# Kernel optimization log

Measured on AMD Instinct MI355X. Metric: run time of the kernel, lower is better.

## Reference

```python
import jax, jax.numpy as jnp
import numpy as np

B, L, H, V = 16, 1024, 512, 32000
HALF = H // 2
ALPHA = 0.95
EPS_NORM = 1e-12
EPS_LN = 1e-5


def setup_inputs() -> dict:
    key = jax.random.key(0)
    ks = jax.random.split(key, 12)
    s = 0.02
    return {
        "seq": jax.random.randint(ks[0], (B, L), 0, V),
        "embed": jax.random.normal(ks[1], (V, H), jnp.float32) * s,
        "ff_w1": jax.random.normal(ks[2], (2 * H, H), jnp.float32) * s,
        "ff_b1": jnp.zeros((2 * H,), jnp.float32),
        "ff_w2": jax.random.normal(ks[3], (H, 2 * H), jnp.float32) * s,
        "ff_b2": jnp.zeros((H,), jnp.float32),
        "gamma": jnp.ones((H,), jnp.float32),
        "beta": jnp.zeros((H,), jnp.float32),
        "sem_w": jax.random.normal(ks[4], (HALF, H), jnp.float32) * s,
        "epi_w": jax.random.normal(ks[5], (HALF, H), jnp.float32) * s,
        "rp_w": jax.random.normal(ks[6], (H, H), jnp.float32) * s,
        "rp_b": jnp.zeros((H,), jnp.float32),
        "out_w": jax.random.normal(ks[7], (V, H), jnp.float32) * s,
        "out_b": jnp.zeros((V,), jnp.float32),
    }


def _layernorm(x, gamma, beta):
    mu = jnp.mean(x, axis=-1, keepdims=True)
    var = jnp.mean(jnp.square(x - mu), axis=-1, keepdims=True)
    return (x - mu) * jax.lax.rsqrt(var + EPS_LN) * gamma + beta


def _l2norm(k):
    # F.normalize: k / max(||k||_2, eps)
    n = jnp.sqrt(jnp.sum(jnp.square(k), axis=-1, keepdims=True))
    return k / jnp.maximum(n, EPS_NORM)


def reference(seq, embed, ff_w1, ff_b1, ff_w2, ff_b2, gamma, beta,
              sem_w, epi_w, rp_w, rp_b, out_w, out_b):
    h = embed[seq]  # [B, L, H]
    ff = jnp.maximum(jnp.einsum('blh,fh->blf', h, ff_w1) + ff_b1, 0.0)
    ff = jnp.einsum('blf,hf->blh', ff, ff_w2) + ff_b2
    h = _layernorm(h + ff, gamma, beta)  # [B, L, H]

    # precompute all keys, time-major for scan: [L, B, half]
    ks_all = jnp.einsum('blh,ch->lbc', h, sem_w)
    ke_all = jnp.einsum('blh,ch->lbc', h, epi_w)

    def step(carry, inp):
        Ms, Me = carry                      # [B, half, half]
        ks, ke = inp                        # [B, half]
        kns = _l2norm(ks)
        kne = _l2norm(ke)
        vps = jnp.einsum('bij,bj->bi', Ms, kns)
        vpe = jnp.einsum('bij,bj->bi', Me, kne)
        Ds = (ks - vps)[:, :, None] * kns[:, None, :]
        De = (ke - vpe)[:, :, None] * kne[:, None, :]
        Ms = Ms + (1.0 - ALPHA) * Ds
        Me = Me + (1.0 - ALPHA) * De
        return (Ms, Me), None

    M0 = jnp.zeros((B, HALF, HALF), h.dtype)
    (M_s, M_e), _ = jax.lax.scan(step, (M0, M0), (ks_all[:L - 1], ke_all[:L - 1]))

    qs = ks_all[L - 1]  # sem_p(h[:, -1])
    qe = ke_all[L - 1]  # epi_p(h[:, -1])
    cs = jnp.einsum('bij,bj->bi', M_s, qs)
    ce = jnp.einsum('bij,bj->bi', M_e, qe)
    c = jnp.concatenate([cs, ce], axis=-1)  # [B, H]
    r = jnp.einsum('bh,gh->bg', c, rp_w) + rp_b
    return jnp.einsum('bh,vh->bv', r, out_w) + out_b  # [B, V]
```

## Files before the change

kernel.cpp:

```cpp
#include <hip/hip_runtime.h>
#include <stdint.h>

#define Bsz 16
#define Lsz 1024
#define Hsz 512
#define Vsz 32000
#define HALF 256
#define BETA 0.05f

typedef unsigned short u16;
typedef __attribute__((ext_vector_type(8))) short short8;
typedef __attribute__((ext_vector_type(4))) float f32x4;

__device__ __forceinline__ float bf2f(u16 u) { return __uint_as_float(((unsigned int)u) << 16); }
__device__ __forceinline__ u16 f2bf(float f) {
    unsigned int u = __float_as_uint(f);
    return (u16)((u + 0x7FFFu + ((u >> 16) & 1u)) >> 16);
}
__device__ __forceinline__ bool mode_f32(const void* gamma) {
    return *(const unsigned int*)gamma == 0x3F800000u;
}

__device__ __forceinline__ float wave_sum(float p) {
    p += __shfl_xor(p, 32, 64);
    p += __shfl_xor(p, 16, 64);
    p += __shfl_xor(p, 8, 64);
    p += __shfl_xor(p, 4, 64);
    p += __shfl_xor(p, 2, 64);
    p += __shfl_xor(p, 1, 64);
    return p;
}

__device__ __forceinline__ void cvt8(const void* src, u16* dst, int i, bool f32m) {
    union { u16 u[8]; uint4 q; } o;
    if (f32m) {
        const float* s = (const float*)src + i;
        const float4 a = *(const float4*)s;
        const float4 b = *(const float4*)(s + 4);
        o.u[0] = f2bf(a.x); o.u[1] = f2bf(a.y); o.u[2] = f2bf(a.z); o.u[3] = f2bf(a.w);
        o.u[4] = f2bf(b.x); o.u[5] = f2bf(b.y); o.u[6] = f2bf(b.z); o.u[7] = f2bf(b.w);
    } else {
        o.q = *(const uint4*)((const u16*)src + i);
    }
    *(uint4*)(dst + i) = o.q;
}

__global__ __launch_bounds__(256)
void cvt_all(const void* s0, const void* s1, const void* s2, const void* s3,
             const void* s4, const void* s5, const void* s6, const void* s7,
             const void* s8, const void* s9, const void* s10,
             u16* d0, u16* d1, u16* d2, u16* d3, u16* d4, u16* d5, u16* d6,
             u16* d7, u16* d8, u16* d9, u16* d10, const void* gamma) {
    const bool f32m = mode_f32(gamma);
    const int g = blockIdx.x * 256 + threadIdx.x;
    const void* src; u16* dst; int off;
    if      (g < 65536)  { src = s0;  dst = d0;  off = g; }
    else if (g < 131072) { src = s1;  dst = d1;  off = g - 65536; }
    else if (g < 147456) { src = s2;  dst = d2;  off = g - 131072; }
    else if (g < 163840) { src = s3;  dst = d3;  off = g - 147456; }
    else if (g < 196608) { src = s4;  dst = d4;  off = g - 163840; }
    else if (g < 196736) { src = s5;  dst = d5;  off = g - 196608; }
    else if (g < 196800) { src = s6;  dst = d6;  off = g - 196736; }
    else if (g < 196864) { src = s7;  dst = d7;  off = g - 196800; }
    else if (g < 196928) { src = s8;  dst = d8;  off = g - 196864; }
    else if (g < 196992) { src = s9;  dst = d9;  off = g - 196928; }
    else if (g < 200992) { src = s10; dst = d10; off = g - 196992; }
    else return;
    cvt8(src, dst, off * 8, f32m);
}

__global__ __launch_bounds__(256)
void gather_kernel(const int* __restrict__ seq, const void* __restrict__ embed,
                   u16* __restrict__ h0, const void* __restrict__ gamma) {
    const bool f32m = mode_f32(gamma);
    const int row = blockIdx.x * 4 + (threadIdx.x >> 6);
    const int lane = threadIdx.x & 63;
    const int tok = seq[row];
    union { u16 u[8]; uint4 q; } o;
    if (f32m) {
        const float* e = (const float*)embed + (size_t)tok * Hsz + lane * 8;
        const float4 a = *(const float4*)e;
        const float4 b = *(const float4*)(e + 4);
        o.u[0] = f2bf(a.x); o.u[1] = f2bf(a.y); o.u[2] = f2bf(a.z); o.u[3] = f2bf(a.w);
        o.u[4] = f2bf(b.x); o.u[5] = f2bf(b.y); o.u[6] = f2bf(b.z); o.u[7] = f2bf(b.w);
    } else {
        o.q = *((const uint4*)((const u16*)embed + (size_t)tok * Hsz) + lane);
    }
    *((uint4*)(h0 + (size_t)row * Hsz) + lane) = o.q;
}

template <int EPI>
__global__ __launch_bounds__(256)
void gemm128(const u16* __restrict__ A, const u16* __restrict__ B0,
             const u16* __restrict__ B1, const u16* __restrict__ bias,
             const u16* resid, void* Cout, int M, int N, int K) {
    __shared__ u16 Als[128 * 32];
    __shared__ u16 Bls[128 * 32];
    const int tid = threadIdx.x;
    const int wave = tid >> 6, lane = tid & 63;
    const int m0 = blockIdx.y * 128, n0 = blockIdx.x * 128;

    const u16* Bt;
    if (EPI == 2) Bt = (n0 < HALF) ? (B0 + (size_t)n0 * K) : (B1 + (size_t)(n0 - HALF) * K);
    else          Bt = B0 + (size_t)n0 * K;
    const u16* At = A + (size_t)m0 * K;

    const int wm = wave >> 1, wn = wave & 1;
    const int srow = lane >> 2;
    const int sk = (lane & 3) * 8;
    const int fr = lane & 15;
    const int fq = (lane >> 4) * 8;

    f32x4 acc[4][4];
#pragma unroll
    for (int i = 0; i < 4; i++)
#pragma unroll
        for (int j = 0; j < 4; j++) acc[i][j] = (f32x4){0.f, 0.f, 0.f, 0.f};

    for (int k0 = 0; k0 < K; k0 += 32) {
        __syncthreads();
#pragma unroll
        for (int c = 0; c < 2; c++) {
            const int ch = wave * 2 + c;
            const int row = ch * 16 + srow;
            __builtin_amdgcn_global_load_lds(
                (const __attribute__((address_space(1))) uint32_t*)(At + (size_t)row * K + k0 + sk),
                (__attribute__((address_space(3))) uint32_t*)(&Als[ch * 512]), 16, 0, 0);
            __builtin_amdgcn_global_load_lds(
                (const __attribute__((address_space(1))) uint32_t*)(Bt + (size_t)row * K + k0 + sk),
                (__attribute__((address_space(3))) uint32_t*)(&Bls[ch * 512]), 16, 0, 0);
        }
        __syncthreads();
        short8 af[4], bfr[4];
#pragma unroll
        for (int i = 0; i < 4; i++)
            af[i] = *(const short8*)&Als[(wm * 64 + i * 16 + fr) * 32 + fq];
#pragma unroll
        for (int j = 0; j < 4; j++)
            bfr[j] = *(const short8*)&Bls[(wn * 64 + j * 16 + fr) * 32 + fq];
#pragma unroll
        for (int i = 0; i < 4; i++)
#pragma unroll
            for (int j = 0; j < 4; j++)
                acc[i][j] = __builtin_amdgcn_mfma_f32_16x16x32_bf16(af[i], bfr[j], acc[i][j], 0, 0, 0);
    }

#pragma unroll
    for (int i = 0; i < 4; i++) {
#pragma unroll
        for (int j = 0; j < 4; j++) {
            const int n = n0 + wn * 64 + j * 16 + fr;
#pragma unroll
            for (int r = 0; r < 4; r++) {
                const int m = m0 + wm * 64 + i * 16 + (lane >> 4) * 4 + r;
                float v = acc[i][j][r];
                if (EPI == 0) {
                    v += bf2f(bias[n]);
                    v = v > 0.f ? v : 0.f;
                    ((u16*)Cout)[(size_t)m * N + n] = f2bf(v);
                } else if (EPI == 1) {
                    v += bf2f(bias[n]) + bf2f(resid[(size_t)m * N + n]);
                    ((u16*)Cout)[(size_t)m * N + n] = f2bf(v);
                } else {
                    const int mem = n >> 8, col = n & 255;
                    const int b = m >> 10, t = m & 1023;
                    ((u16*)Cout)[((size_t)(mem * Bsz + b) * Lsz + t) * HALF + col] = f2bf(v);
                }
            }
        }
    }
}

__global__ __launch_bounds__(256)
void ln_kernel(const u16* hs, const u16* __restrict__ gamma,
               const u16* __restrict__ beta, u16* hn) {
    const int row = blockIdx.x * 4 + (threadIdx.x >> 6);
    const int lane = threadIdx.x & 63;
    const uint4 raw = *(const uint4*)(hs + (size_t)row * Hsz + lane * 8);
    const u16* xr = (const u16*)&raw;
    float v[8];
#pragma unroll
    for (int j = 0; j < 8; j++) v[j] = bf2f(xr[j]);
    float s = 0.f;
#pragma unroll
    for (int j = 0; j < 8; j++) s += v[j];
    s = wave_sum(s);
    const float mu = s * (1.f / 512.f);
    float q = 0.f;
#pragma unroll
    for (int j = 0; j < 8; j++) { v[j] -= mu; q += v[j] * v[j]; }
    q = wave_sum(q);
    const float rstd = rsqrtf(q * (1.f / 512.f) + 1e-5f);
    union { u16 u[8]; uint4 qv; } o;
#pragma unroll
    for (int j = 0; j < 8; j++) {
        const int n = lane * 8 + j;
        o.u[j] = f2bf(v[j] * rstd * bf2f(gamma[n]) + bf2f(beta[n]));
    }
    *(uint4*)(hn + (size_t)row * Hsz + lane * 8) = o.qv;
}

__global__ __launch_bounds__(256)
void normalize_kernel(u16* kb, float* __restrict__ norms) {
    const int row = blockIdx.x * 4 + (threadIdx.x >> 6);
    const int lane = threadIdx.x & 63;
    u16* p = kb + (size_t)row * HALF + lane * 4;
    uint2 raw = *(uint2*)p;
    const u16* kp = (const u16*)&raw;
    float f[4];
#pragma unroll
    for (int j = 0; j < 4; j++) f[j] = bf2f(kp[j]);
    float s = f[0]*f[0] + f[1]*f[1] + f[2]*f[2] + f[3]*f[3];
    s = wave_sum(s);
    const float n = fmaxf(sqrtf(s), 1e-12f);
    const float inv = 1.f / n;
    union { u16 u[4]; uint2 q; } o;
#pragma unroll
    for (int j = 0; j < 4; j++) o.u[j] = f2bf(f[j] * inv);
    *(uint2*)p = o.q;
    if (lane == 0) norms[row] = n;
}

__global__ __launch_bounds__(256)
void gramsolve_kernel(const u16* __restrict__ kn, float* __restrict__ W0,
                      float* __restrict__ W1) {
    __shared__ u16 ls[64 * 264];
    __shared__ float Gl[64 * 64];
    const int mb = blockIdx.x, c = blockIdx.y;
    const int tid = threadIdx.x;
    const u16* src = kn + ((size_t)mb * Lsz + c * 64) * HALF;
    {
        const int row = tid >> 2, p = tid & 3;
        const u16* sp = src + row * 256 + p * 64;
        u16* dp = ls + row * 264 + p * 64;
#pragma unroll
        for (int i = 0; i < 8; i++)
            *(uint4*)(dp + i * 8) = *(const uint4*)(sp + i * 8);
    }
    __syncthreads();
    const int wave = tid >> 6, lane = tid & 63;
    const int fr = lane & 15, fq = (lane >> 4) * 8;
    f32x4 acc[4];
#pragma unroll
    for (int j = 0; j < 4; j++) acc[j] = (f32x4){0.f, 0.f, 0.f, 0.f};
    for (int k0 = 0; k0 < 256; k0 += 32) {
        const short8 a = *(const short8*)&ls[(wave * 16 + fr) * 264 + k0 + fq];
#pragma unroll
        for (int j = 0; j < 4; j++) {
            const short8 b = *(const short8*)&ls[(j * 16 + fr) * 264 + k0 + fq];
            acc[j] = __builtin_amdgcn_mfma_f32_16x16x32_bf16(a, b, acc[j], 0, 0, 0);
        }
    }
#pragma unroll
    for (int j = 0; j < 4; j++)
#pragma unroll
        for (int r = 0; r < 4; r++)
            Gl[(wave * 16 + (lane >> 4) * 4 + r) * 64 + j * 16 + fr] = acc[j][r];
    __syncthreads();

    float* Wc = (c < 8) ? (W0 + (((size_t)mb * 8 + c) * 64) * HALF)
                        : (W1 + (((size_t)mb * 8 + (c - 8)) * 64) * HALF);
    const bool last = (c == 15);
    float w[64];
#pragma unroll
    for (int t = 63; t >= 0; --t) {
        float a0 = 0.f, a1 = 0.f, a2 = 0.f, a3 = 0.f;
        const int q0 = (t + 4) & ~3;
#pragma unroll
        for (int tp = t + 1; tp < q0; ++tp) a0 += Gl[t * 64 + tp] * w[tp];
#pragma unroll
        for (int q = q0; q < 64; q += 4) {
            const f32x4 g = *(const f32x4*)&Gl[t * 64 + q];
            a0 += g[0] * w[q];     a1 += g[1] * w[q + 1];
            a2 += g[2] * w[q + 2]; a3 += g[3] * w[q + 3];
        }
        float wt = bf2f(ls[t * 264 + tid]) - BETA * ((a0 + a1) + (a2 + a3));
        if (last && t == 63) wt = 0.f;
        w[t] = wt;
        Wc[t * HALF + tid] = wt;
    }
}

__global__ __launch_bounds__(256)
void scan3_kernel(const u16* __restrict__ kn, const float* __restrict__ norms,
                  const float* __restrict__ W0, const float* __restrict__ W1,
                  float* __restrict__ cbuf) {
    __shared__ float uL[256], sL[64], s2L[64];
    const int mb = blockIdx.x;
    const int tid = threadIdx.x;
    const int t = tid >> 2, p = tid & 3;
    const u16* knb = kn + (size_t)mb * Lsz * HALF;
    const float* nb = norms + (size_t)mb * Lsz;

    float u = bf2f(knb[1023 * HALF + tid]) * nb[1023];
    float cacc = 0.f;
    uL[tid] = u;

    f32x4 wr[16], wn[16];
    {
        const float* wp = W1 + (((size_t)mb * 8 + 7) * 64 + t) * HALF + p * 64;
#pragma unroll
        for (int i = 0; i < 16; i++) wr[i] = *(const f32x4*)(wp + i * 4);
    }
    __syncthreads();

    for (int c = 15; c >= 0; --c) {
        {
            float pa = 0.f, pb = 0.f;
#pragma unroll
            for (int i = 0; i < 16; i += 2) {
                const f32x4 u0 = *(const f32x4*)&uL[p * 64 + i * 4];
                const f32x4 u1 = *(const f32x4*)&uL[p * 64 + i * 4 + 4];
                pa += wr[i][0] * u0[0] + wr[i][1] * u0[1]
                    + wr[i][2] * u0[2] + wr[i][3] * u0[3];
                pb += wr[i + 1][0] * u1[0] + wr[i + 1][1] * u1[1]
                    + wr[i + 1][2] * u1[2] + wr[i + 1][3] * u1[3];
            }
            float part = pa + pb;
            part += __shfl_xor(part, 1, 64);
            part += __shfl_xor(part, 2, 64);
            if (p == 0) { sL[t] = part; s2L[t] = part * nb[c * 64 + t]; }
        }
        if (c > 0) {
            const float* wpn = (c - 1 < 8)
                ? (W0 + (((size_t)mb * 8 + (c - 1)) * 64 + t) * HALF + p * 64)
                : (W1 + (((size_t)mb * 8 + (c - 9)) * 64 + t) * HALF + p * 64);
#pragma unroll
            for (int i = 0; i < 16; i++) wn[i] = *(const f32x4*)(wpn + i * 4);
        }
        __syncthreads();
        {
            const u16* kcol = knb + (size_t)c * 64 * HALF + tid;
            float du0 = 0.f, du1 = 0.f, dc0 = 0.f, dc1 = 0.f;
#pragma unroll
            for (int tq = 0; tq < 16; tq++) {
                const f32x4 sv  = *(const f32x4*)&sL[tq * 4];
                const f32x4 s2v = *(const f32x4*)&s2L[tq * 4];
                const float k0v = bf2f(kcol[(size_t)(tq * 4 + 0) * HALF]);
                const float k1v = bf2f(kcol[(size_t)(tq * 4 + 1) * HALF]);
                const float k2v = bf2f(kcol[(size_t)(tq * 4 + 2) * HALF]);
                const float k3v = bf2f(kcol[(size_t)(tq * 4 + 3) * HALF]);
                du0 += sv[0] * k0v + sv[1] * k1v;
                du1 += sv[2] * k2v + sv[3] * k3v;
                dc0 += s2v[0] * k0v + s2v[1] * k1v;
                dc1 += s2v[2] * k2v + s2v[3] * k3v;
            }
            u -= BETA * (du0 + du1);
            cacc += BETA * (dc0 + dc1);
            uL[tid] = u;
        }
        __syncthreads();
        if (c > 0) {
#pragma unroll
            for (int i = 0; i < 16; i++) wr[i] = wn[i];
        }
    }
    const int b = mb & 15, mem = mb >> 4;
    cbuf[(size_t)b * Hsz + mem * HALF + tid] = cacc;
}

__global__ __launch_bounds__(256)
void rproj_kernel(const float* __restrict__ cbuf, const u16* __restrict__ rpw,
                  const u16* __restrict__ rpb, u16* __restrict__ rbuf) {
    __shared__ float cl[Hsz];
    const int b = blockIdx.x, tid = threadIdx.x;
    cl[tid] = cbuf[(size_t)b * Hsz + tid];
    cl[tid + 256] = cbuf[(size_t)b * Hsz + 256 + tid];
    __syncthreads();
#pragma unroll
    for (int gg = 0; gg < 2; gg++) {
        const int g = gg * 256 + tid;
        const u16* wr = rpw + (size_t)g * Hsz;
        float acc = bf2f(rpb[g]);
        for (int k = 0; k < Hsz; k += 8) {
            const uint4 w8 = *(const uint4*)(wr + k);
            const u16* w = (const u16*)&w8;
            const float4 c0 = *(const float4*)&cl[k];
            const float4 c1 = *(const float4*)&cl[k + 4];
            acc += bf2f(w[0]) * c0.x + bf2f(w[1]) * c0.y + bf2f(w[2]) * c0.z + bf2f(w[3]) * c0.w
                 + bf2f(w[4]) * c1.x + bf2f(w[5]) * c1.y + bf2f(w[6]) * c1.z + bf2f(w[7]) * c1.w;
        }
        rbuf[(size_t)b * Hsz + g] = f2bf(acc);
    }
}

__global__ __launch_bounds__(256)
void logits_kernel(const u16* __restrict__ rbuf, const void* __restrict__ outw,
                   const u16* __restrict__ outb, void* __restrict__ out,
                   const void* __restrict__ gamma) {
    __shared__ u16 rls[16 * Hsz];
    const bool f32m = mode_f32(gamma);
    const int tid = threadIdx.x;
    {
        const uint4* src = (const uint4*)rbuf;
        uint4* dst = (uint4*)rls;
#pragma unroll
        for (int i = 0; i < 4; i++) dst[i * 256 + tid] = src[i * 256 + tid];
    }
    __syncthreads();
    const int wave = tid >> 6, lane = tid & 63;
    const int n0 = blockIdx.x * 256 + wave * 64;
    const int fr = lane & 15, fq = (lane >> 4) * 8;
    f32x4 acc[4];
#pragma unroll
    for (int j = 0; j < 4; j++) acc[j] = (f32x4){0.f, 0.f, 0.f, 0.f};
    if (f32m) {
        for (int k0 = 0; k0 < Hsz; k0 += 32) {
            const short8 af = *(const short8*)&rls[fr * Hsz + k0 + fq];
#pragma unroll
            for (int j = 0; j < 4; j++) {
                const float* wp = (const float*)outw + (size_t)(n0 + j * 16 + fr) * Hsz + k0 + fq;
                const float4 a = *(const float4*)wp;
                const float4 bq = *(const float4*)(wp + 4);
                union { u16 u[8]; short8 v; } bb;
                bb.u[0] = f2bf(a.x); bb.u[1] = f2bf(a.y); bb.u[2] = f2bf(a.z); bb.u[3] = f2bf(a.w);
                bb.u[4] = f2bf(bq.x); bb.u[5] = f2bf(bq.y); bb.u[6] = f2bf(bq.z); bb.u[7] = f2bf(bq.w);
                acc[j] = __builtin_amdgcn_mfma_f32_16x16x32_bf16(af, bb.v, acc[j], 0, 0, 0);
            }
        }
    } else {
        for (int k0 = 0; k0 < Hsz; k0 += 32) {
            const short8 af = *(const short8*)&rls[fr * Hsz + k0 + fq];
#pragma unroll
            for (int j = 0; j < 4; j++) {
                const short8 b8 = *(const short8*)((const u16*)outw + (size_t)(n0 + j * 16 + fr) * Hsz + k0 + fq);
                acc[j] = __builtin_amdgcn_mfma_f32_16x16x32_bf16(af, b8, acc[j], 0, 0, 0);
            }
        }
    }
#pragma unroll
    for (int j = 0; j < 4; j++) {
        const int v = n0 + j * 16 + fr;
        const float bv = bf2f(outb[v]);
#pragma unroll
        for (int r = 0; r < 4; r++) {
            const int bb = (lane >> 4) * 4 + r;
            const float val = acc[j][r] + bv;
            if (f32m) ((float*)out)[(size_t)bb * Vsz + v] = val;
            else      ((u16*)out)[(size_t)bb * Vsz + v] = f2bf(val);
        }
    }
}

extern "C" void kernel_launch(void* const* d_in, const int* in_sizes, int n_in,
                              void* d_out, int out_size, void* d_ws, size_t ws_size,
                              hipStream_t stream) {
    const int*  seq   = (const int*)d_in[0];
    const void* embed = d_in[1];
    const void* ffw1  = d_in[2];
    const void* ffb1  = d_in[3];
    const void* ffw2  = d_in[4];
    const void* ffb2  = d_in[5];
    const void* gamma = d_in[6];
    const void* beta  = d_in[7];
    const void* semw  = d_in[8];
    const void* epiw  = d_in[9];
    const void* rpw   = d_in[10];
    const void* rpb   = d_in[11];
    const void* outw  = d_in[12];
    const void* outb  = d_in[13];

    char* ws = (char*)d_ws;
    u16*   h0    = (u16*)(ws + 0);
    u16*   C1    = (u16*)(ws + (size_t)0x1000000);
    u16*   kbuf  = (u16*)(ws + (size_t)0x1000000);
    float* W0    = (float*)(ws + 0);
    float* W1    = (float*)(ws + (size_t)0x2000000);
    size_t off   = 50331648;
    float* norms = (float*)(ws + off); off += (size_t)32 * Lsz * 4;
    u16* cffw1 = (u16*)(ws + off); off += (size_t)1024 * 512 * 2;
    u16* cffw2 = (u16*)(ws + off); off += (size_t)512 * 1024 * 2;
    u16* csemw = (u16*)(ws + off); off += (size_t)256 * 512 * 2;
    u16* cepiw = (u16*)(ws + off); off += (size_t)256 * 512 * 2;
    u16* crpw  = (u16*)(ws + off); off += (size_t)512 * 512 * 2;
    u16* cffb1 = (u16*)(ws + off); off += 1024 * 2;
    u16* cffb2 = (u16*)(ws + off); off += 512 * 2;
    u16* cgam  = (u16*)(ws + off); off += 512 * 2;
    u16* cbet  = (u16*)(ws + off); off += 512 * 2;
    u16* crpb  = (u16*)(ws + off); off += 512 * 2;
    u16* coutb = (u16*)(ws + off); off += (size_t)32000 * 2;
    off = (off + 255) & ~(size_t)255;
    float* cbuf = (float*)(ws + off); off += (size_t)16 * 512 * 4;
    u16*   rbuf = (u16*)(ws + off);

    cvt_all<<<786, 256, 0, stream>>>(ffw1, ffw2, semw, epiw, rpw, ffb1, ffb2,
                                     gamma, beta, rpb, outb,
                                     cffw1, cffw2, csemw, cepiw, crpw, cffb1, cffb2,
                                     cgam, cbet, crpb, coutb, gamma);
    gather_kernel<<<4096, 256, 0, stream>>>(seq, embed, h0, gamma);
    gemm128<0><<<dim3(8, 128), 256, 0, stream>>>(h0, cffw1, nullptr, cffb1, nullptr, C1,
                                                 16384, 1024, 512);
    gemm128<1><<<dim3(4, 128), 256, 0, stream>>>(C1, cffw2, nullptr, cffb2, h0, h0,
                                                 16384, 512, 1024);
    ln_kernel<<<4096, 256, 0, stream>>>(h0, cgam, cbet, h0);
    gemm128<2><<<dim3(4, 128), 256, 0, stream>>>(h0, csemw, cepiw, nullptr, nullptr, kbuf,
                                                 16384, 512, 512);
    normalize_kernel<<<8192, 256, 0, stream>>>(kbuf, norms);
    gramsolve_kernel<<<dim3(32, 16), 256, 0, stream>>>(kbuf, W0, W1);
    scan3_kernel<<<32, 256, 0, stream>>>(kbuf, norms, W0, W1, cbuf);
    rproj_kernel<<<16, 256, 0, stream>>>(cbuf, crpw, crpb, rbuf);
    logits_kernel<<<125, 256, 0, stream>>>(rbuf, outw, coutb, d_out, gamma);
}
```

Measured before the change: 394.9 us.

## Store W in fp16 and add transposed key copy for contiguous scan reads

The key-projection GEMM now also writes a transposed [mem,b,col,t] copy of the raw keys, so the serial scan kernel can load each thread's 64-key chunk as contiguous uint4 vectors instead of strided scalar loads. The gramsolve W matrices are stored as fp16 instead of fp32, halving the bytes the scan streams per chunk. The normalize step now also stores the inverse norms, and the scan uses them to rescale the raw transposed keys. This trades an extra strided 8-byte store in the GEMM epilogue and reduced W precision for less memory traffic in the latency-bound 32-block scan.

```diff
diff --git a/kernel.cpp b/kernel.cpp
--- a/kernel.cpp
+++ b/kernel.cpp
@@ -16,6 +16,10 @@
 __device__ __forceinline__ u16 f2bf(float f) {
     unsigned int u = __float_as_uint(f);
     return (u16)((u + 0x7FFFu + ((u >> 16) & 1u)) >> 16);
+}
+__device__ __forceinline__ u16 f2h(float f) {
+    _Float16 h = (_Float16)f;
+    return *(u16*)&h;
 }
 __device__ __forceinline__ bool mode_f32(const void* gamma) {
     return *(const unsigned int*)gamma == 0x3F800000u;
@@ -93,7 +97,8 @@
 __global__ __launch_bounds__(256)
 void gemm128(const u16* __restrict__ A, const u16* __restrict__ B0,
              const u16* __restrict__ B1, const u16* __restrict__ bias,
-             const u16* resid, void* Cout, int M, int N, int K) {
+             const u16* resid, void* Cout, u16* __restrict__ kT,
+             int M, int N, int K) {
     __shared__ u16 Als[128 * 32];
     __shared__ u16 Bls[128 * 32];
     const int tid = threadIdx.x;
@@ -150,21 +155,32 @@
 #pragma unroll
         for (int j = 0; j < 4; j++) {
             const int n = n0 + wn * 64 + j * 16 + fr;
-#pragma unroll
-            for (int r = 0; r < 4; r++) {
-                const int m = m0 + wm * 64 + i * 16 + (lane >> 4) * 4 + r;
-                float v = acc[i][j][r];
-                if (EPI == 0) {
-                    v += bf2f(bias[n]);
-                    v = v > 0.f ? v : 0.f;
-                    ((u16*)Cout)[(size_t)m * N + n] = f2bf(v);
-                } else if (EPI == 1) {
-                    v += bf2f(bias[n]) + bf2f(resid[(size_t)m * N + n]);
-                    ((u16*)Cout)[(size_t)m * N + n] = f2bf(v);
-                } else {
-                    const int mem = n >> 8, col = n & 255;
-                    const int b = m >> 10, t = m & 1023;
-                    ((u16*)Cout)[((size_t)(mem * Bsz + b) * Lsz + t) * HALF + col] = f2bf(v);
+            if (EPI == 2) {
+                const int mbase = m0 + wm * 64 + i * 16 + (lane >> 4) * 4;
+                const int mem = n >> 8, col = n & 255;
+                const int b = mbase >> 10, t0 = mbase & 1023;
+                u16 tv[4];
+#pragma unroll
+                for (int r = 0; r < 4; r++) {
+                    const int t = t0 + r;
+                    const u16 bv = f2bf(acc[i][j][r]);
+                    tv[r] = bv;
+                    ((u16*)Cout)[((size_t)(mem * Bsz + b) * Lsz + t) * HALF + col] = bv;
+                }
+                *(uint2*)&kT[((size_t)(mem * Bsz + b) * HALF + col) * Lsz + t0] = *(uint2*)tv;
+            } else {
+#pragma unroll
+                for (int r = 0; r < 4; r++) {
+                    const int m = m0 + wm * 64 + i * 16 + (lane >> 4) * 4 + r;
+                    float v = acc[i][j][r];
+                    if (EPI == 0) {
+                        v += bf2f(bias[n]);
+                        v = v > 0.f ? v : 0.f;
+                        ((u16*)Cout)[(size_t)m * N + n] = f2bf(v);
+                    } else {
+                        v += bf2f(bias[n]) + bf2f(resid[(size_t)m * N + n]);
+                        ((u16*)Cout)[(size_t)m * N + n] = f2bf(v);
+                    }
                 }
             }
         }
@@ -201,7 +217,7 @@
 }
 
 __global__ __launch_bounds__(256)
-void normalize_kernel(u16* kb, float* __restrict__ norms) {
+void normalize_kernel(u16* kb, float* __restrict__ norms, float* __restrict__ invs) {
     const int row = blockIdx.x * 4 + (threadIdx.x >> 6);
     const int lane = threadIdx.x & 63;
     u16* p = kb + (size_t)row * HALF + lane * 4;
@@ -218,12 +234,11 @@
 #pragma unroll
     for (int j = 0; j < 4; j++) o.u[j] = f2bf(f[j] * inv);
     *(uint2*)p = o.q;
-    if (lane == 0) norms[row] = n;
-}
-
-__global__ __launch_bounds__(256)
-void gramsolve_kernel(const u16* __restrict__ kn, float* __restrict__ W0,
-                      float* __restrict__ W1) {
+    if (lane == 0) { norms[row] = n; invs[row] = inv; }
+}
+
+__global__ __launch_bounds__(256)
+void gramsolve_kernel(const u16* __restrict__ kn, u16* __restrict__ W) {
     __shared__ u16 ls[64 * 264];
     __shared__ float Gl[64 * 64];
     const int mb = blockIdx.x, c = blockIdx.y;
@@ -258,8 +273,7 @@
             Gl[(wave * 16 + (lane >> 4) * 4 + r) * 64 + j * 16 + fr] = acc[j][r];
     __syncthreads();
 
-    float* Wc = (c < 8) ? (W0 + (((size_t)mb * 8 + c) * 64) * HALF)
-                        : (W1 + (((size_t)mb * 8 + (c - 8)) * 64) * HALF);
+    u16* Wc = W + (((size_t)mb * 16 + c) * 64) * HALF;
     const bool last = (c == 15);
     float w[64];
 #pragma unroll
@@ -277,30 +291,33 @@
         float wt = bf2f(ls[t * 264 + tid]) - BETA * ((a0 + a1) + (a2 + a3));
         if (last && t == 63) wt = 0.f;
         w[t] = wt;
-        Wc[t * HALF + tid] = wt;
-    }
-}
-
-__global__ __launch_bounds__(256)
-void scan3_kernel(const u16* __restrict__ kn, const float* __restrict__ norms,
-                  const float* __restrict__ W0, const float* __restrict__ W1,
-                  float* __restrict__ cbuf) {
-    __shared__ float uL[256], sL[64], s2L[64];
+        Wc[t * HALF + tid] = f2h(wt);
+    }
+}
+
+__global__ __launch_bounds__(256, 1)
+void scan3_kernel(const u16* __restrict__ kn, const u16* __restrict__ kT,
+                  const float* __restrict__ norms, const float* __restrict__ invs,
+                  const u16* __restrict__ W, float* __restrict__ cbuf) {
+    __shared__ float uL[256], suL[64], scL[64];
     const int mb = blockIdx.x;
     const int tid = threadIdx.x;
     const int t = tid >> 2, p = tid & 3;
-    const u16* knb = kn + (size_t)mb * Lsz * HALF;
     const float* nb = norms + (size_t)mb * Lsz;
-
-    float u = bf2f(knb[1023 * HALF + tid]) * nb[1023];
+    const float* ib = invs + (size_t)mb * Lsz;
+
+    float u = bf2f(kn[((size_t)mb * Lsz + 1023) * HALF + tid]) * nb[1023];
     float cacc = 0.f;
     uL[tid] = u;
 
-    f32x4 wr[16], wn[16];
+    const u16* kTrow = kT + ((size_t)mb * HALF + tid) * Lsz;
+    const u16* Wb = W + (size_t)mb * 16 * 64 * HALF;
+
+    uint4 wr[8], wn[8];
     {
-        const float* wp = W1 + (((size_t)mb * 8 + 7) * 64 + t) * HALF + p * 64;
-#pragma unroll
-        for (int i = 0; i < 16; i++) wr[i] = *(const f32x4*)(wp + i * 4);
+        const u16* wp = Wb + ((size_t)15 * 64 + t) * HALF + p * 64;
+#pragma unroll
+        for (int i = 0; i < 8; i++) wr[i] = *(const uint4*)(wp + i * 8);
     }
     __syncthreads();
 
@@ -308,42 +325,47 @@
         {
             float pa = 0.f, pb = 0.f;
 #pragma unroll
-            for (int i = 0; i < 16; i += 2) {
-                const f32x4 u0 = *(const f32x4*)&uL[p * 64 + i * 4];
-                const f32x4 u1 = *(const f32x4*)&uL[p * 64 + i * 4 + 4];
-                pa += wr[i][0] * u0[0] + wr[i][1] * u0[1]
-                    + wr[i][2] * u0[2] + wr[i][3] * u0[3];
-                pb += wr[i + 1][0] * u1[0] + wr[i + 1][1] * u1[1]
-                    + wr[i + 1][2] * u1[2] + wr[i + 1][3] * u1[3];
+            for (int i = 0; i < 8; i++) {
+                union { uint4 q; _Float16 h[8]; } wv; wv.q = wr[i];
+                const f32x4 u0 = *(const f32x4*)&uL[p * 64 + i * 8];
+                const f32x4 u1 = *(const f32x4*)&uL[p * 64 + i * 8 + 4];
+                pa += (float)wv.h[0] * u0[0] + (float)wv.h[1] * u0[1]
+                    + (float)wv.h[2] * u0[2] + (float)wv.h[3] * u0[3];
+                pb += (float)wv.h[4] * u1[0] + (float)wv.h[5] * u1[1]
+                    + (float)wv.h[6] * u1[2] + (float)wv.h[7] * u1[3];
             }
             float part = pa + pb;
             part += __shfl_xor(part, 1, 64);
             part += __shfl_xor(part, 2, 64);
-            if (p == 0) { sL[t] = part; s2L[t] = part * nb[c * 64 + t]; }
+            if (p == 0) { suL[t] = part * ib[c * 64 + t]; scL[t] = part; }
         }
         if (c > 0) {
-            const float* wpn = (c - 1 < 8)
-                ? (W0 + (((size_t)mb * 8 + (c - 1)) * 64 + t) * HALF + p * 64)
-                : (W1 + (((size_t)mb * 8 + (c - 9)) * 64 + t) * HALF + p * 64);
-#pragma unroll
-            for (int i = 0; i < 16; i++) wn[i] = *(const f32x4*)(wpn + i * 4);
+            const u16* wpn = Wb + ((size_t)(c - 1) * 64 + t) * HALF + p * 64;
+#pragma unroll
+            for (int i = 0; i < 8; i++) wn[i] = *(const uint4*)(wpn + i * 8);
         }
         __syncthreads();
         {
-            const u16* kcol = knb + (size_t)c * 64 * HALF + tid;
+            const u16* kp = kTrow + c * 64;
+            uint4 kq[8];
+#pragma unroll
+            for (int i = 0; i < 8; i++) kq[i] = *(const uint4*)(kp + i * 8);
             float du0 = 0.f, du1 = 0.f, dc0 = 0.f, dc1 = 0.f;
 #pragma unroll
-            for (int tq = 0; tq < 16; tq++) {
-                const f32x4 sv  = *(const f32x4*)&sL[tq * 4];
-                const f32x4 s2v = *(const f32x4*)&s2L[tq * 4];
-                const float k0v = bf2f(kcol[(size_t)(tq * 4 + 0) * HALF]);
-                const float k1v = bf2f(kcol[(size_t)(tq * 4 + 1) * HALF]);
-                const float k2v = bf2f(kcol[(size_t)(tq * 4 + 2) * HALF]);
-                const float k3v = bf2f(kcol[(size_t)(tq * 4 + 3) * HALF]);
-                du0 += sv[0] * k0v + sv[1] * k1v;
-                du1 += sv[2] * k2v + sv[3] * k3v;
-                dc0 += s2v[0] * k0v + s2v[1] * k1v;
-                dc1 += s2v[2] * k2v + s2v[3] * k3v;
+            for (int i = 0; i < 8; i++) {
+                const u16* kk = (const u16*)&kq[i];
+                const f32x4 sa = *(const f32x4*)&suL[i * 8];
+                const f32x4 sb = *(const f32x4*)&suL[i * 8 + 4];
+                const f32x4 ca = *(const f32x4*)&scL[i * 8];
+                const f32x4 cb = *(const f32x4*)&scL[i * 8 + 4];
+                const float k0 = bf2f(kk[0]), k1 = bf2f(kk[1]);
+                const float k2 = bf2f(kk[2]), k3 = bf2f(kk[3]);
+                const float k4 = bf2f(kk[4]), k5 = bf2f(kk[5]);
+                const float k6 = bf2f(kk[6]), k7 = bf2f(kk[7]);
+                du0 += sa[0] * k0 + sa[1] * k1 + sa[2] * k2 + sa[3] * k3;
+                du1 += sb[0] * k4 + sb[1] * k5 + sb[2] * k6 + sb[3] * k7;
+                dc0 += ca[0] * k0 + ca[1] * k1 + ca[2] * k2 + ca[3] * k3;
+                dc1 += cb[0] * k4 + cb[1] * k5 + cb[2] * k6 + cb[3] * k7;
             }
             u -= BETA * (du0 + du1);
             cacc += BETA * (dc0 + dc1);
@@ -352,7 +374,7 @@
         __syncthreads();
         if (c > 0) {
 #pragma unroll
-            for (int i = 0; i < 16; i++) wr[i] = wn[i];
+            for (int i = 0; i < 8; i++) wr[i] = wn[i];
         }
     }
     const int b = mb & 15, mem = mb >> 4;
@@ -462,12 +484,13 @@
 
     char* ws = (char*)d_ws;
     u16*   h0    = (u16*)(ws + 0);
+    u16*   Wbuf  = (u16*)(ws + 0);
     u16*   C1    = (u16*)(ws + (size_t)0x1000000);
     u16*   kbuf  = (u16*)(ws + (size_t)0x1000000);
-    float* W0    = (float*)(ws + 0);
-    float* W1    = (float*)(ws + (size_t)0x2000000);
+    u16*   kT    = (u16*)(ws + (size_t)0x2000000);
     size_t off   = 50331648;
     float* norms = (float*)(ws + off); off += (size_t)32 * Lsz * 4;
+    float* invs  = (float*)(ws + off); off += (size_t)32 * Lsz * 4;
     u16* cffw1 = (u16*)(ws + off); off += (size_t)1024 * 512 * 2;
     u16* cffw2 = (u16*)(ws + off); off += (size_t)512 * 1024 * 2;
     u16* csemw = (u16*)(ws + off); off += (size_t)256 * 512 * 2;
@@ -489,15 +512,15 @@
                                      cgam, cbet, crpb, coutb, gamma);
     gather_kernel<<<4096, 256, 0, stream>>>(seq, embed, h0, gamma);
     gemm128<0><<<dim3(8, 128), 256, 0, stream>>>(h0, cffw1, nullptr, cffb1, nullptr, C1,
-                                                 16384, 1024, 512);
+                                                 nullptr, 16384, 1024, 512);
     gemm128<1><<<dim3(4, 128), 256, 0, stream>>>(C1, cffw2, nullptr, cffb2, h0, h0,
-                                                 16384, 512, 1024);
+                                                 nullptr, 16384, 512, 1024);
     ln_kernel<<<4096, 256, 0, stream>>>(h0, cgam, cbet, h0);
     gemm128<2><<<dim3(4, 128), 256, 0, stream>>>(h0, csemw, cepiw, nullptr, nullptr, kbuf,
-                                                 16384, 512, 512);
-    normalize_kernel<<<8192, 256, 0, stream>>>(kbuf, norms);
-    gramsolve_kernel<<<dim3(32, 16), 256, 0, stream>>>(kbuf, W0, W1);
-    scan3_kernel<<<32, 256, 0, stream>>>(kbuf, norms, W0, W1, cbuf);
+                                                 kT, 16384, 512, 512);
+    normalize_kernel<<<8192, 256, 0, stream>>>(kbuf, norms, invs);
+    gramsolve_kernel<<<dim3(32, 16), 256, 0, stream>>>(kbuf, Wbuf);
+    scan3_kernel<<<32, 256, 0, stream>>>(kbuf, kT, norms, invs, Wbuf, cbuf);
     rproj_kernel<<<16, 256, 0, stream>>>(cbuf, crpw, crpb, rbuf);
     logits_kernel<<<125, 256, 0, stream>>>(rbuf, outw, coutb, d_out, gamma);
 }
```

Measured after the change: 384.6 us. -2.6%, faster.
